# Optimization experiments

Hardware: AMD Instinct MI355X
Metric: run time of the kernel (lower is better)

The kernel has to match this reference:

```python
import jax, jax.numpy as jnp
import numpy as np

HEADS = 8
EPS = 1e-5


def layernorm(x, g, b):
    mu = jnp.mean(x, axis=-1, keepdims=True)
    var = jnp.mean((x - mu) ** 2, axis=-1, keepdims=True)
    return (x - mu) * jax.lax.rsqrt(var + EPS) * g + b


def setup_inputs() -> dict:
    key = jax.random.key(0)
    ks = jax.random.split(key, 5)
    B, C, H, W = 8, 384, 32, 32
    d = C
    s = 0.02
    return {
        "x": jax.random.normal(ks[0], (B, C, H, W), jnp.float32),
        "ln1_g": jnp.ones((d,), jnp.float32),
        "ln1_b": jnp.zeros((d,), jnp.float32),
        "lna_g": jnp.ones((d,), jnp.float32),
        "lna_b": jnp.zeros((d,), jnp.float32),
        "w_qkv": jax.random.normal(ks[1], (d, 3 * d), jnp.float32) * s,
        "w_out": jax.random.normal(ks[2], (d, d), jnp.float32) * s,
        "ln2_g": jnp.ones((d,), jnp.float32),
        "ln2_b": jnp.zeros((d,), jnp.float32),
        "w1": jax.random.normal(ks[3], (d, 4 * d), jnp.float32) * s,
        "b1": jnp.zeros((4 * d,), jnp.float32),
        "w2": jax.random.normal(ks[4], (4 * d, d), jnp.float32) * s,
        "b2": jnp.zeros((d,), jnp.float32),
    }


def reference(x, ln1_g, ln1_b, lna_g, lna_b, w_qkv, w_out, ln2_g, ln2_b, w1, b1, w2, b2):
    B, C, H, W = x.shape
    d = C
    dh = d // HEADS
    scale = dh ** (-0.5)
    # flatten spatial -> tokens: [B, N, C]
    t = x.reshape(B, C, H * W).transpose(0, 2, 1)

    # --- attention branch (note: double pre-norm, as in original) ---
    a = layernorm(t, ln1_g, ln1_b)
    a = layernorm(a, lna_g, lna_b)
    qkv = a @ w_qkv  # [B, N, 3d]
    q, k, v = jnp.split(qkv, 3, axis=-1)
    q = q.reshape(B, -1, HEADS, dh).transpose(0, 2, 1, 3)  # b h n d
    k = k.reshape(B, -1, HEADS, dh).transpose(0, 2, 1, 3)
    v = v.reshape(B, -1, HEADS, dh).transpose(0, 2, 1, 3)
    dots = jnp.einsum("bhnd,bhmd->bhnm", q, k) * scale
    attn = jax.nn.softmax(dots, axis=-1)
    o = jnp.einsum("bhnm,bhmd->bhnd", attn, v)
    o = o.transpose(0, 2, 1, 3).reshape(B, -1, d)
    t = t + o @ w_out

    # --- MLP branch (exact GELU, as torch nn.GELU default) ---
    m = layernorm(t, ln2_g, ln2_b)
    m = jax.nn.gelu(m @ w1 + b1, approximate=False) @ w2 + b2
    t = t + m

    return t.transpose(0, 2, 1).reshape(B, C, H, W)
```

## Files before the change

### kernel.cpp

```cpp
#include <hip/hip_runtime.h>
#include <math.h>

#define NTOK 1024
#define DM   384
#define NHEAD 8
#define DH   48
#define BATCH 8
#define NROWS (BATCH * NTOK)
#define SC2   (0.14433756729740643f * 1.4426950408889634f)

typedef __attribute__((ext_vector_type(8))) _Float16 f16x8;
typedef __attribute__((ext_vector_type(2))) __fp16 fp16x2_raw;
typedef __attribute__((ext_vector_type(4))) float f32x4;

#define ASYNC16(gp, lp) __builtin_amdgcn_global_load_lds( \
    (const __attribute__((address_space(1))) void*)(gp),  \
    (__attribute__((address_space(3))) void*)(lp), 16, 0, 0)

__device__ __forceinline__ unsigned int pkh(float a, float b) {
    union { fp16x2_raw h; unsigned int u; } cv;
    cv.h = __builtin_amdgcn_cvt_pkrtz(a, b);
    return cv.u;
}

__device__ __forceinline__ float gelu_fast(float v) {
    const float u = v * (0.7978845608f + 0.0356774081f * v * v);
    const float e = exp2f(u * 2.885390082f);
    return v * e / (e + 1.0f);
}

__global__ __launch_bounds__(256) void prep_kernel(const float* __restrict__ x,
                                                   const float* __restrict__ ln1_g,
                                                   const float* __restrict__ ln1_b,
                                                   const float* __restrict__ lna_g,
                                                   const float* __restrict__ lna_b,
                                                   float* __restrict__ t,
                                                   _Float16* __restrict__ a_h,
                                                   const float* __restrict__ wqkv,
                                                   const float* __restrict__ wout,
                                                   const float* __restrict__ w1,
                                                   const float* __restrict__ w2,
                                                   _Float16* __restrict__ wqkvT,
                                                   _Float16* __restrict__ woutT,
                                                   _Float16* __restrict__ w1T,
                                                   _Float16* __restrict__ w2T) {
    __shared__ float Ts[32][389];
    const int bid = blockIdx.x;
    const int tid = threadIdx.x;

    if (bid >= 256) {
        float (*tile)[33] = (float(*)[33])&Ts[0][0];
        const int wb = bid - 256;
        const float* W; _Float16* Wt; int K, N, nx, tt;
        if (wb < 432)       { W = wqkv; Wt = wqkvT; K = 384;  N = 1152; nx = 36; tt = wb; }
        else if (wb < 576)  { W = wout; Wt = woutT; K = 384;  N = 384;  nx = 12; tt = wb - 432; }
        else if (wb < 1152) { W = w1;   Wt = w1T;   K = 384;  N = 1536; nx = 48; tt = wb - 576; }
        else                { W = w2;   Wt = w2T;   K = 1536; N = 384;  nx = 12; tt = wb - 1152; }
        const int n0 = (tt % nx) * 32, k0 = (tt / nx) * 32;
        const int tx = tid & 31, ty = tid >> 5;
        #pragma unroll
        for (int i = ty; i < 32; i += 8)
            tile[i][tx] = W[(size_t)(k0 + i) * N + n0 + tx];
        __syncthreads();
        #pragma unroll
        for (int i = ty; i < 32; i += 8)
            Wt[(size_t)(n0 + i) * K + k0 + tx] = (_Float16)tile[tx][i];
        return;
    }

    const int b = bid >> 5, n0 = (bid & 31) * 32;
    const int tx = tid & 31, ty8 = tid >> 5;
    const float* xb = x + (size_t)b * (DM * NTOK);
    #pragma unroll
    for (int c0 = 0; c0 < DM; c0 += 32) {
        #pragma unroll
        for (int i = ty8; i < 32; i += 8)
            Ts[tx][c0 + i] = xb[(size_t)(c0 + i) * NTOK + n0 + tx];
    }
    __syncthreads();

    const int g = tid >> 3, sub = tid & 7;
    const int c0 = sub * 48;
    float xv[48];
    #pragma unroll
    for (int k = 0; k < 12; ++k)
        *(float4*)&xv[k * 4] = *(const float4*)&Ts[g][c0 + k * 4];

    const size_t trow = (size_t)((b << 10) + n0 + g) * DM;
    float s = 0.0f, sq = 0.0f;
    #pragma unroll
    for (int k = 0; k < 12; ++k)
        *(float4*)&t[trow + c0 + k * 4] = *(const float4*)&xv[k * 4];
    #pragma unroll
    for (int j = 0; j < 48; ++j) { s += xv[j]; sq += xv[j] * xv[j]; }
    s += __shfl_xor(s, 1, 64); sq += __shfl_xor(sq, 1, 64);
    s += __shfl_xor(s, 2, 64); sq += __shfl_xor(sq, 2, 64);
    s += __shfl_xor(s, 4, 64); sq += __shfl_xor(sq, 4, 64);
    float mu = s * (1.0f / DM);
    float var = fmaxf(sq * (1.0f / DM) - mu * mu, 0.0f);
    float r1 = rsqrtf(var + 1e-5f);

    float s2 = 0.0f, q2 = 0.0f;
    #pragma unroll
    for (int k = 0; k < 12; ++k) {
        const float4 gk = *(const float4*)&ln1_g[c0 + k * 4];
        const float4 bk = *(const float4*)&ln1_b[c0 + k * 4];
        float y0 = (xv[k*4+0] - mu) * r1 * gk.x + bk.x;
        float y1 = (xv[k*4+1] - mu) * r1 * gk.y + bk.y;
        float y2 = (xv[k*4+2] - mu) * r1 * gk.z + bk.z;
        float y3 = (xv[k*4+3] - mu) * r1 * gk.w + bk.w;
        xv[k*4+0] = y0; xv[k*4+1] = y1; xv[k*4+2] = y2; xv[k*4+3] = y3;
        s2 += (y0 + y1) + (y2 + y3);
        q2 += (y0*y0 + y1*y1) + (y2*y2 + y3*y3);
    }
    s2 += __shfl_xor(s2, 1, 64); q2 += __shfl_xor(q2, 1, 64);
    s2 += __shfl_xor(s2, 2, 64); q2 += __shfl_xor(q2, 2, 64);
    s2 += __shfl_xor(s2, 4, 64); q2 += __shfl_xor(q2, 4, 64);
    mu = s2 * (1.0f / DM);
    var = fmaxf(q2 * (1.0f / DM) - mu * mu, 0.0f);
    const float r2 = rsqrtf(var + 1e-5f);

    unsigned int d[12];
    #pragma unroll
    for (int k = 0; k < 12; ++k) {
        const float4 gk = *(const float4*)&lna_g[c0 + k * 4];
        const float4 bk = *(const float4*)&lna_b[c0 + k * 4];
        const float y0 = (xv[k*4+0] - mu) * r2 * gk.x + bk.x;
        const float y1 = (xv[k*4+1] - mu) * r2 * gk.y + bk.y;
        const float y2 = (xv[k*4+2] - mu) * r2 * gk.z + bk.z;
        const float y3 = (xv[k*4+3] - mu) * r2 * gk.w + bk.w;
        d[k*2+0] = pkh(y0, y1); d[k*2+1] = pkh(y2, y3);
    }
    unsigned int* op = (unsigned int*)(a_h + trow + c0);
    #pragma unroll
    for (int k = 0; k < 3; ++k)
        *(uint4*)(op + k * 4) = *(const uint4*)&d[k * 4];
}

__global__ __launch_bounds__(256) void ln2_kernel(const float* __restrict__ in,
                                                  const float* __restrict__ gg,
                                                  const float* __restrict__ bb,
                                                  _Float16* __restrict__ outp) {
    const int row = blockIdx.x * 4 + (threadIdx.x >> 6);
    const int lane = threadIdx.x & 63;
    const float* ip = in + (size_t)row * DM + lane * 6;
    float v[6];
    *(float2*)&v[0] = *(const float2*)(ip);
    *(float2*)&v[2] = *(const float2*)(ip + 2);
    *(float2*)&v[4] = *(const float2*)(ip + 4);
    float s = 0.0f, sq = 0.0f;
    #pragma unroll
    for (int j = 0; j < 6; ++j) { s += v[j]; sq += v[j] * v[j]; }
    #pragma unroll
    for (int off = 1; off < 64; off <<= 1) {
        s += __shfl_xor(s, off, 64);
        sq += __shfl_xor(sq, off, 64);
    }
    const float mu = s * (1.0f / DM);
    const float var = fmaxf(sq * (1.0f / DM) - mu * mu, 0.0f);
    const float rs = rsqrtf(var + 1e-5f);
    const float* gp = gg + lane * 6;
    const float* bp = bb + lane * 6;
    float y[6];
    #pragma unroll
    for (int j = 0; j < 6; ++j) y[j] = (v[j] - mu) * rs * gp[j] + bp[j];
    unsigned int* op = (unsigned int*)(outp + (size_t)row * DM + lane * 6);
    op[0] = pkh(y[0], y[1]); op[1] = pkh(y[2], y[3]); op[2] = pkh(y[4], y[5]);
}

template <int EPI, int BN>
__global__ __launch_bounds__(256) void gemm_f16(const _Float16* __restrict__ A,
                                                const _Float16* __restrict__ Bt,
                                                const float* __restrict__ bias,
                                                const float* __restrict__ R,
                                                _Float16* __restrict__ Ch,
                                                float* __restrict__ Cf,
                                                int M, int N, int K) {
    constexpr int NFRAG = BN / 32;
    constexpr int BSTG = BN / 32;
    __shared__ _Float16 As[2][128][64];
    __shared__ _Float16 Bs[2][BN][64];
    const int tid = threadIdx.x;
    const int w = tid >> 6, lane = tid & 63;
    const int l15 = lane & 15, lq = lane >> 4;
    const int bm = blockIdx.y * 128, bn = blockIdx.x * BN;
    const int moff = (w & 1) * 64, noff = (w >> 1) * (BN / 2);

    const int srw = lane >> 3, pp = lane & 7;
    const int c = pp ^ srw;
    const _Float16* Ag[4];
    const _Float16* Bg[BSTG];
    #pragma unroll
    for (int j = 0; j < 4; ++j)
        Ag[j] = A + (size_t)(bm + w * 32 + j * 8 + srw) * K + c * 8;
    #pragma unroll
    for (int j = 0; j < BSTG; ++j)
        Bg[j] = Bt + (size_t)(bn + w * (BN / 4) + j * 8 + srw) * K + c * 8;

    const int octA = ((lq ^ (l15 & 7)) << 4);

    f32x4 acc[4][NFRAG];
    #pragma unroll
    for (int mi = 0; mi < 4; ++mi)
        #pragma unroll
        for (int ni = 0; ni < NFRAG; ++ni) acc[mi][ni] = (f32x4){0.f, 0.f, 0.f, 0.f};

    #pragma unroll
    for (int j = 0; j < 4; ++j) { ASYNC16(Ag[j], &As[0][w * 32 + j * 8][0]); Ag[j] += 64; }
    #pragma unroll
    for (int j = 0; j < BSTG; ++j) { ASYNC16(Bg[j], &Bs[0][w * (BN / 4) + j * 8][0]); Bg[j] += 64; }

    int cur = 0;
    for (int k0 = 64; k0 <= K; k0 += 64) {
        __syncthreads();
        if (k0 < K) {
            #pragma unroll
            for (int j = 0; j < 4; ++j) { ASYNC16(Ag[j], &As[cur ^ 1][w * 32 + j * 8][0]); Ag[j] += 64; }
            #pragma unroll
            for (int j = 0; j < BSTG; ++j) { ASYNC16(Bg[j], &Bs[cur ^ 1][w * (BN / 4) + j * 8][0]); Bg[j] += 64; }
        }
        const char* Ab = (const char*)&As[cur][0][0];
        const char* Bb = (const char*)&Bs[cur][0][0];
        #pragma unroll
        for (int ks = 0; ks < 2; ++ks) {
            const int ox = octA ^ (ks << 6);
            f16x8 af[4], bfr[NFRAG];
            #pragma unroll
            for (int mi = 0; mi < 4; ++mi)
                af[mi] = *(const f16x8*)(Ab + ((moff + mi * 16 + l15) << 7) + ox);
            #pragma unroll
            for (int ni = 0; ni < NFRAG; ++ni)
                bfr[ni] = *(const f16x8*)(Bb + ((noff + ni * 16 + l15) << 7) + ox);
            #pragma unroll
            for (int mi = 0; mi < 4; ++mi)
                #pragma unroll
                for (int ni = 0; ni < NFRAG; ++ni)
                    acc[mi][ni] = __builtin_amdgcn_mfma_f32_16x16x32_f16(af[mi], bfr[ni], acc[mi][ni], 0, 0, 0);
        }
        cur ^= 1;
    }

    #pragma unroll
    for (int mi = 0; mi < 4; ++mi) {
        #pragma unroll
        for (int ni = 0; ni < NFRAG; ++ni) {
            const int col = bn + noff + ni * 16 + l15;
            float bv = 0.0f;
            if (EPI >= 2) bv = bias[col];
            if (EPI == 4) {
                const int row0 = bm + moff + mi * 16 + lq * 4;
                const int b = row0 >> 10, nn = row0 & 1023;
                float4 vv;
                vv.x = acc[mi][ni][0] + bv + R[(size_t)(row0 + 0) * N + col];
                vv.y = acc[mi][ni][1] + bv + R[(size_t)(row0 + 1) * N + col];
                vv.z = acc[mi][ni][2] + bv + R[(size_t)(row0 + 2) * N + col];
                vv.w = acc[mi][ni][3] + bv + R[(size_t)(row0 + 3) * N + col];
                *(float4*)(Cf + (size_t)b * (DM * NTOK) + (size_t)col * NTOK + nn) = vv;
            } else {
                #pragma unroll
                for (int r = 0; r < 4; ++r) {
                    const int row = bm + moff + mi * 16 + lq * 4 + r;
                    const size_t idx = (size_t)row * N + col;
                    float v = acc[mi][ni][r];
                    if (EPI == 2) v = gelu_fast(v + bv);
                    if (EPI == 0 || EPI == 2) Ch[idx] = (_Float16)v;
                    else                      Cf[idx] = v + R[idx];
                }
            }
        }
    }
}

__global__ __launch_bounds__(256) void attn_kernel(const _Float16* __restrict__ qkv,
                                                   _Float16* __restrict__ o) {
    __shared__ _Float16 Ks[2][64][64];
    __shared__ _Float16 Vt[2][48][72];
    __shared__ _Float16 Ps[4][32][72];

    const int tid = threadIdx.x;
    const int w = tid >> 6, lane = tid & 63;
    const int l15 = lane & 15, lq = lane >> 4;
    const int bid = blockIdx.x;
    const int bh = ((bid >> 3) & 7) * 8 + (bid & 7);
    const int qt0 = (bid >> 6) * 128;
    const int h = bh & 7, b = bh >> 3;

    const _Float16* qbase = qkv + (size_t)b * NTOK * 1152 + h * 48;
    const _Float16* kbase = qbase + 384;
    const _Float16* vbase = qbase + 768;

    f16x8 qf[2][2];
    #pragma unroll
    for (int qi = 0; qi < 2; ++qi) {
        const size_t qrow = (size_t)(qt0 + w * 32 + qi * 16 + l15) * 1152;
        #pragma unroll
        for (int ks = 0; ks < 2; ++ks) {
            if (ks == 0 || lq < 2)
                qf[qi][ks] = *(const f16x8*)(qbase + qrow + ks * 32 + lq * 8);
            else
                qf[qi][ks] = (f16x8){(_Float16)0, (_Float16)0, (_Float16)0, (_Float16)0,
                                     (_Float16)0, (_Float16)0, (_Float16)0, (_Float16)0};
        }
    }

    const int srw = lane >> 3, pp = lane & 7;
    const int ck = pp ^ srw;
    const int ckoff = (ck < 6) ? ck * 8 : (ck - 6) * 8;
    const _Float16* Kg = kbase + (size_t)(w * 16 + srw) * 1152 + ckoff;
    const int vtp = tid & 31, vfo = tid >> 5;
    const _Float16* Vg = vbase + (size_t)(vtp * 2) * 1152 + vfo * 8;

    const int octK = ((lq ^ (l15 & 7)) << 4);

    ASYNC16(Kg, &Ks[0][w * 16][0]);
    ASYNC16(Kg + 8 * 1152, &Ks[0][w * 16 + 8][0]);
    Kg += 64 * 1152;
    uint4 va, vb;
    if (vfo < 6) { va = *(const uint4*)Vg; vb = *(const uint4*)(Vg + 1152); }
    Vg += 64 * 1152;

    f32x4 oacc[2][3];
    float lpart[2] = {0.0f, 0.0f};
    #pragma unroll
    for (int qi = 0; qi < 2; ++qi)
        #pragma unroll
        for (int vf = 0; vf < 3; ++vf) oacc[qi][vf] = (f32x4){0.f, 0.f, 0.f, 0.f};

    int cur = 0;
    for (int kt = 0; kt < 16; ++kt) {
        if (vfo < 6) {
            const unsigned short* as = (const unsigned short*)&va;
            const unsigned short* bs = (const unsigned short*)&vb;
            #pragma unroll
            for (int j = 0; j < 8; ++j) {
                const unsigned int dw = (unsigned int)as[j] | ((unsigned int)bs[j] << 16);
                *(unsigned int*)((char*)&Vt[cur][0][0] + (vfo * 8 + j) * 144 + vtp * 4) = dw;
            }
        }
        __syncthreads();
        if (kt < 15) {
            ASYNC16(Kg, &Ks[cur ^ 1][w * 16][0]);
            ASYNC16(Kg + 8 * 1152, &Ks[cur ^ 1][w * 16 + 8][0]);
            Kg += 64 * 1152;
            if (vfo < 6) { va = *(const uint4*)Vg; vb = *(const uint4*)(Vg + 1152); }
            Vg += 64 * 1152;
        }

        f32x4 sacc[2][4];
        #pragma unroll
        for (int qi = 0; qi < 2; ++qi)
            #pragma unroll
            for (int mi = 0; mi < 4; ++mi) sacc[qi][mi] = (f32x4){0.f, 0.f, 0.f, 0.f};
        #pragma unroll
        for (int ks = 0; ks < 2; ++ks) {
            const int ox = octK ^ (ks << 6);
            #pragma unroll
            for (int mi = 0; mi < 4; ++mi) {
                const f16x8 kf = *(const f16x8*)((const char*)&Ks[cur][0][0] + ((mi * 16 + l15) << 7) + ox);
                sacc[0][mi] = __builtin_amdgcn_mfma_f32_16x16x32_f16(kf, qf[0][ks], sacc[0][mi], 0, 0, 0);
                sacc[1][mi] = __builtin_amdgcn_mfma_f32_16x16x32_f16(kf, qf[1][ks], sacc[1][mi], 0, 0, 0);
            }
        }

        #pragma unroll
        for (int qi = 0; qi < 2; ++qi) {
            #pragma unroll
            for (int mi = 0; mi < 4; ++mi) {
                const float p0 = exp2f(sacc[qi][mi][0] * SC2);
                const float p1 = exp2f(sacc[qi][mi][1] * SC2);
                const float p2 = exp2f(sacc[qi][mi][2] * SC2);
                const float p3 = exp2f(sacc[qi][mi][3] * SC2);
                lpart[qi] += (p0 + p1) + (p2 + p3);
                uint2 d;
                d.x = pkh(p0, p1); d.y = pkh(p2, p3);
                *(uint2*)((char*)&Ps[w][0][0] + (qi * 16 + l15) * 144 + (mi * 16 + lq * 4) * 2) = d;
            }
        }
        asm volatile("s_waitcnt lgkmcnt(0)" ::: "memory");

        #pragma unroll
        for (int ks = 0; ks < 2; ++ks) {
            const int kk2 = ks * 64 + lq * 16;
            const f16x8 pf0 = *(const f16x8*)((const char*)&Ps[w][0][0] + l15 * 144 + kk2);
            const f16x8 pf1 = *(const f16x8*)((const char*)&Ps[w][0][0] + (16 + l15) * 144 + kk2);
            #pragma unroll
            for (int vf = 0; vf < 3; ++vf) {
                const f16x8 vv = *(const f16x8*)((const char*)&Vt[cur][0][0] + (vf * 16 + l15) * 144 + kk2);
                oacc[0][vf] = __builtin_amdgcn_mfma_f32_16x16x32_f16(vv, pf0, oacc[0][vf], 0, 0, 0);
                oacc[1][vf] = __builtin_amdgcn_mfma_f32_16x16x32_f16(vv, pf1, oacc[1][vf], 0, 0, 0);
            }
        }
        cur ^= 1;
    }

    #pragma unroll
    for (int qi = 0; qi < 2; ++qi) {
        float ls = lpart[qi];
        ls += __shfl_xor(ls, 16, 64);
        ls += __shfl_xor(ls, 32, 64);
        const float linv = 1.0f / ls;
        _Float16* ob = o + (size_t)(b * NTOK + qt0 + w * 32 + qi * 16 + l15) * DM + h * DH;
        #pragma unroll
        for (int vf = 0; vf < 3; ++vf) {
            uint2 d;
            d.x = pkh(oacc[qi][vf][0] * linv, oacc[qi][vf][1] * linv);
            d.y = pkh(oacc[qi][vf][2] * linv, oacc[qi][vf][3] * linv);
            *(uint2*)(ob + vf * 16 + lq * 4) = d;
        }
    }
}

extern "C" void kernel_launch(void* const* d_in, const int* in_sizes, int n_in,
                              void* d_out, int out_size, void* d_ws, size_t ws_size,
                              hipStream_t stream) {
    const float* x     = (const float*)d_in[0];
    const float* ln1_g = (const float*)d_in[1];
    const float* ln1_b = (const float*)d_in[2];
    const float* lna_g = (const float*)d_in[3];
    const float* lna_b = (const float*)d_in[4];
    const float* w_qkv = (const float*)d_in[5];
    const float* w_out = (const float*)d_in[6];
    const float* ln2_g = (const float*)d_in[7];
    const float* ln2_b = (const float*)d_in[8];
    const float* w1    = (const float*)d_in[9];
    const float* b1    = (const float*)d_in[10];
    const float* w2    = (const float*)d_in[11];
    const float* b2    = (const float*)d_in[12];
    float* out = (float*)d_out;

    char* wsb = (char*)d_ws;
    float* t          = (float*)(wsb);
    _Float16* a_h     = (_Float16*)(wsb + 12582912);
    _Float16* qkv_h   = (_Float16*)(wsb + 18874368);
    _Float16* o_h     = (_Float16*)(wsb + 37748736);
    _Float16* h1_h    = (_Float16*)(wsb + 44040192);
    _Float16* wqkvT   = (_Float16*)(wsb + 69206016);
    _Float16* woutT   = (_Float16*)(wsb + 70090752);
    _Float16* w1T     = (_Float16*)(wsb + 70385664);
    _Float16* w2T     = (_Float16*)(wsb + 71565312);

    prep_kernel<<<256 + 1728, 256, 0, stream>>>(x, ln1_g, ln1_b, lna_g, lna_b, t, a_h,
                                                w_qkv, w_out, w1, w2, wqkvT, woutT, w1T, w2T);
    gemm_f16<0, 128><<<dim3(9, 64), 256, 0, stream>>>(a_h, wqkvT, nullptr, nullptr, qkv_h, nullptr, NROWS, 3 * DM, DM);
    attn_kernel<<<512, 256, 0, stream>>>(qkv_h, o_h);
    gemm_f16<1, 64><<<dim3(6, 64), 256, 0, stream>>>(o_h, woutT, nullptr, t, nullptr, t, NROWS, DM, DM);
    ln2_kernel<<<2048, 256, 0, stream>>>(t, ln2_g, ln2_b, a_h);
    gemm_f16<2, 128><<<dim3(12, 64), 256, 0, stream>>>(a_h, w1T, b1, nullptr, h1_h, nullptr, NROWS, 4 * DM, DM);
    gemm_f16<4, 64><<<dim3(6, 64), 256, 0, stream>>>(h1_h, w2T, b2, t, nullptr, out, NROWS, DM, 4 * DM);
}
```

Measured before the change: 234.6 us.

## Split-K the final MLP GEMM with merge kernel and halve attention query tile

```diff
diff --git a/kernel.cpp b/kernel.cpp
--- a/kernel.cpp
+++ b/kernel.cpp
@@ -186,16 +186,19 @@
     const int bm = blockIdx.y * 128, bn = blockIdx.x * BN;
     const int moff = (w & 1) * 64, noff = (w >> 1) * (BN / 2);
 
+    const int kspan = (EPI == 5) ? (K >> 1) : K;
+    const int zoff = (EPI == 5) ? blockIdx.z * kspan : 0;
+
     const int srw = lane >> 3, pp = lane & 7;
     const int c = pp ^ srw;
     const _Float16* Ag[4];
     const _Float16* Bg[BSTG];
     #pragma unroll
     for (int j = 0; j < 4; ++j)
-        Ag[j] = A + (size_t)(bm + w * 32 + j * 8 + srw) * K + c * 8;
+        Ag[j] = A + (size_t)(bm + w * 32 + j * 8 + srw) * K + zoff + c * 8;
     #pragma unroll
     for (int j = 0; j < BSTG; ++j)
-        Bg[j] = Bt + (size_t)(bn + w * (BN / 4) + j * 8 + srw) * K + c * 8;
+        Bg[j] = Bt + (size_t)(bn + w * (BN / 4) + j * 8 + srw) * K + zoff + c * 8;
 
     const int octA = ((lq ^ (l15 & 7)) << 4);
 
@@ -211,9 +214,9 @@
     for (int j = 0; j < BSTG; ++j) { ASYNC16(Bg[j], &Bs[0][w * (BN / 4) + j * 8][0]); Bg[j] += 64; }
 
     int cur = 0;
-    for (int k0 = 64; k0 <= K; k0 += 64) {
+    for (int k0 = 64; k0 <= kspan; k0 += 64) {
         __syncthreads();
-        if (k0 < K) {
+        if (k0 < kspan) {
             #pragma unroll
             for (int j = 0; j < 4; ++j) { ASYNC16(Ag[j], &As[cur ^ 1][w * 32 + j * 8][0]); Ag[j] += 64; }
             #pragma unroll
@@ -240,67 +243,72 @@
         cur ^= 1;
     }
 
+    float* Cfz = (EPI == 5) ? (Cf + (size_t)blockIdx.z * NROWS * 384) : Cf;
     #pragma unroll
     for (int mi = 0; mi < 4; ++mi) {
         #pragma unroll
         for (int ni = 0; ni < NFRAG; ++ni) {
             const int col = bn + noff + ni * 16 + l15;
             float bv = 0.0f;
-            if (EPI >= 2) bv = bias[col];
-            if (EPI == 4) {
-                const int row0 = bm + moff + mi * 16 + lq * 4;
-                const int b = row0 >> 10, nn = row0 & 1023;
-                float4 vv;
-                vv.x = acc[mi][ni][0] + bv + R[(size_t)(row0 + 0) * N + col];
-                vv.y = acc[mi][ni][1] + bv + R[(size_t)(row0 + 1) * N + col];
-                vv.z = acc[mi][ni][2] + bv + R[(size_t)(row0 + 2) * N + col];
-                vv.w = acc[mi][ni][3] + bv + R[(size_t)(row0 + 3) * N + col];
-                *(float4*)(Cf + (size_t)b * (DM * NTOK) + (size_t)col * NTOK + nn) = vv;
-            } else {
-                #pragma unroll
-                for (int r = 0; r < 4; ++r) {
-                    const int row = bm + moff + mi * 16 + lq * 4 + r;
-                    const size_t idx = (size_t)row * N + col;
-                    float v = acc[mi][ni][r];
-                    if (EPI == 2) v = gelu_fast(v + bv);
-                    if (EPI == 0 || EPI == 2) Ch[idx] = (_Float16)v;
-                    else                      Cf[idx] = v + R[idx];
-                }
+            if (EPI == 2) bv = bias[col];
+            #pragma unroll
+            for (int r = 0; r < 4; ++r) {
+                const int row = bm + moff + mi * 16 + lq * 4 + r;
+                const size_t idx = (size_t)row * N + col;
+                float v = acc[mi][ni][r];
+                if (EPI == 2) v = gelu_fast(v + bv);
+                if (EPI == 0 || EPI == 2) Ch[idx] = (_Float16)v;
+                else if (EPI == 1)        Cf[idx] = v + R[idx];
+                else                      Cfz[idx] = v;
             }
         }
     }
+}
+
+__global__ __launch_bounds__(256) void merge_kernel(const float* __restrict__ p0,
+                                                    const float* __restrict__ p1,
+                                                    const float* __restrict__ t,
+                                                    const float* __restrict__ b2,
+                                                    float* __restrict__ out) {
+    __shared__ float tile[32][33];
+    const int b = blockIdx.z, n0 = blockIdx.y * 32, c0 = blockIdx.x * 32;
+    const int tx = threadIdx.x & 31, ty = threadIdx.x >> 5;
+    const float bv = b2[c0 + tx];
+    #pragma unroll
+    for (int i = ty; i < 32; i += 8) {
+        const size_t idx = (size_t)((b << 10) + n0 + i) * DM + c0 + tx;
+        tile[i][tx] = p0[idx] + p1[idx] + t[idx] + bv;
+    }
+    __syncthreads();
+    #pragma unroll
+    for (int i = ty; i < 32; i += 8)
+        out[(size_t)b * (DM * NTOK) + (size_t)(c0 + i) * NTOK + n0 + tx] = tile[tx][i];
 }
 
 __global__ __launch_bounds__(256) void attn_kernel(const _Float16* __restrict__ qkv,
                                                    _Float16* __restrict__ o) {
     __shared__ _Float16 Ks[2][64][64];
     __shared__ _Float16 Vt[2][48][72];
-    __shared__ _Float16 Ps[4][32][72];
-
+    __shared__ _Float16 Ps[4][16][72];
     const int tid = threadIdx.x;
     const int w = tid >> 6, lane = tid & 63;
     const int l15 = lane & 15, lq = lane >> 4;
     const int bid = blockIdx.x;
     const int bh = ((bid >> 3) & 7) * 8 + (bid & 7);
-    const int qt0 = (bid >> 6) * 128;
+    const int qt0 = (bid >> 6) * 64;
     const int h = bh & 7, b = bh >> 3;
 
     const _Float16* qbase = qkv + (size_t)b * NTOK * 1152 + h * 48;
     const _Float16* kbase = qbase + 384;
     const _Float16* vbase = qbase + 768;
 
-    f16x8 qf[2][2];
-    #pragma unroll
-    for (int qi = 0; qi < 2; ++qi) {
-        const size_t qrow = (size_t)(qt0 + w * 32 + qi * 16 + l15) * 1152;
-        #pragma unroll
-        for (int ks = 0; ks < 2; ++ks) {
-            if (ks == 0 || lq < 2)
-                qf[qi][ks] = *(const f16x8*)(qbase + qrow + ks * 32 + lq * 8);
-            else
-                qf[qi][ks] = (f16x8){(_Float16)0, (_Float16)0, (_Float16)0, (_Float16)0,
-                                     (_Float16)0, (_Float16)0, (_Float16)0, (_Float16)0};
-        }
+    f16x8 qf[2];
+    {
+        const size_t qrow = (size_t)(qt0 + w * 16 + l15) * 1152;
+        qf[0] = *(const f16x8*)(qbase + qrow + lq * 8);
+        if (lq < 2) qf[1] = *(const f16x8*)(qbase + qrow + 32 + lq * 8);
+        else        qf[1] = (f16x8){(_Float16)0, (_Float16)0, (_Float16)0, (_Float16)0,
+                                    (_Float16)0, (_Float16)0, (_Float16)0, (_Float16)0};
     }
 
     const int srw = lane >> 3, pp = lane & 7;
@@ -319,12 +327,10 @@
     if (vfo < 6) { va = *(const uint4*)Vg; vb = *(const uint4*)(Vg + 1152); }
     Vg += 64 * 1152;
 
-    f32x4 oacc[2][3];
-    float lpart[2] = {0.0f, 0.0f};
-    #pragma unroll
-    for (int qi = 0; qi < 2; ++qi)
-        #pragma unroll
-        for (int vf = 0; vf < 3; ++vf) oacc[qi][vf] = (f32x4){0.f, 0.f, 0.f, 0.f};
+    f32x4 oacc[3];
+    float lpart = 0.0f;
+    #pragma unroll
+    for (int vf = 0; vf < 3; ++vf) oacc[vf] = (f32x4){0.f, 0.f, 0.f, 0.f};
 
     int cur = 0;
     for (int kt = 0; kt < 16; ++kt) {
@@ -346,67 +352,55 @@
             Vg += 64 * 1152;
         }
 
-        f32x4 sacc[2][4];
-        #pragma unroll
-        for (int qi = 0; qi < 2; ++qi)
-            #pragma unroll
-            for (int mi = 0; mi < 4; ++mi) sacc[qi][mi] = (f32x4){0.f, 0.f, 0.f, 0.f};
+        f32x4 sacc[4];
+        #pragma unroll
+        for (int mi = 0; mi < 4; ++mi) sacc[mi] = (f32x4){0.f, 0.f, 0.f, 0.f};
         #pragma unroll
         for (int ks = 0; ks < 2; ++ks) {
             const int ox = octK ^ (ks << 6);
             #pragma unroll
             for (int mi = 0; mi < 4; ++mi) {
                 const f16x8 kf = *(const f16x8*)((const char*)&Ks[cur][0][0] + ((mi * 16 + l15) << 7) + ox);
-                sacc[0][mi] = __builtin_amdgcn_mfma_f32_16x16x32_f16(kf, qf[0][ks], sacc[0][mi], 0, 0, 0);
-                sacc[1][mi] = __builtin_amdgcn_mfma_f32_16x16x32_f16(kf, qf[1][ks], sacc[1][mi], 0, 0, 0);
+                sacc[mi] = __builtin_amdgcn_mfma_f32_16x16x32_f16(kf, qf[ks], sacc[mi], 0, 0, 0);
             }
         }
 
         #pragma unroll
-        for (int qi = 0; qi < 2; ++qi) {
-            #pragma unroll
-            for (int mi = 0; mi < 4; ++mi) {
-                const float p0 = exp2f(sacc[qi][mi][0] * SC2);
-                const float p1 = exp2f(sacc[qi][mi][1] * SC2);
-                const float p2 = exp2f(sacc[qi][mi][2] * SC2);
-                const float p3 = exp2f(sacc[qi][mi][3] * SC2);
-                lpart[qi] += (p0 + p1) + (p2 + p3);
-                uint2 d;
-                d.x = pkh(p0, p1); d.y = pkh(p2, p3);
-                *(uint2*)((char*)&Ps[w][0][0] + (qi * 16 + l15) * 144 + (mi * 16 + lq * 4) * 2) = d;
-            }
+        for (int mi = 0; mi < 4; ++mi) {
+            const float p0 = exp2f(sacc[mi][0] * SC2);
+            const float p1 = exp2f(sacc[mi][1] * SC2);
+            const float p2 = exp2f(sacc[mi][2] * SC2);
+            const float p3 = exp2f(sacc[mi][3] * SC2);
+            lpart += (p0 + p1) + (p2 + p3);
+            uint2 d;
+            d.x = pkh(p0, p1); d.y = pkh(p2, p3);
+            *(uint2*)((char*)&Ps[w][0][0] + l15 * 144 + (mi * 16 + lq * 4) * 2) = d;
         }
         asm volatile("s_waitcnt lgkmcnt(0)" ::: "memory");
 
         #pragma unroll
         for (int ks = 0; ks < 2; ++ks) {
             const int kk2 = ks * 64 + lq * 16;
-            const f16x8 pf0 = *(const f16x8*)((const char*)&Ps[w][0][0] + l15 * 144 + kk2);
-            const f16x8 pf1 = *(const f16x8*)((const char*)&Ps[w][0][0] + (16 + l15) * 144 + kk2);
+            const f16x8 pf = *(const f16x8*)((const char*)&Ps[w][0][0] + l15 * 144 + kk2);
             #pragma unroll
             for (int vf = 0; vf < 3; ++vf) {
                 const f16x8 vv = *(const f16x8*)((const char*)&Vt[cur][0][0] + (vf * 16 + l15) * 144 + kk2);
-                oacc[0][vf] = __builtin_amdgcn_mfma_f32_16x16x32_f16(vv, pf0, oacc[0][vf], 0, 0, 0);
-                oacc[1][vf] = __builtin_amdgcn_mfma_f32_16x16x32_f16(vv, pf1, oacc[1][vf], 0, 0, 0);
+                oacc[vf] = __builtin_amdgcn_mfma_f32_16x16x32_f16(vv, pf, oacc[vf], 0, 0, 0);
             }
         }
         cur ^= 1;
     }
 
-    #pragma unroll
-    for (int qi = 0; qi < 2; ++qi) {
-        float ls = lpart[qi];
-        ls += __shfl_xor(ls, 16, 64);
-        ls += __shfl_xor(ls, 32, 64);
-        const float linv = 1.0f / ls;
-        _Float16* ob = o + (size_t)(b * NTOK + qt0 + w * 32 + qi * 16 + l15) * DM + h * DH;
-        #pragma unroll
-        for (int vf = 0; vf < 3; ++vf) {
-            uint2 d;
-            d.x = pkh(oacc[qi][vf][0] * linv, oacc[qi][vf][1] * linv);
-            d.y = pkh(oacc[qi][vf][2] * linv, oacc[qi][vf][3] * linv);
-            *(uint2*)(ob + vf * 16 + lq * 4) = d;
-        }
+    lpart += __shfl_xor(lpart, 16, 64);
+    lpart += __shfl_xor(lpart, 32, 64);
+    const float linv = 1.0f / lpart;
+    _Float16* ob = o + (size_t)(b * NTOK + qt0 + w * 16 + l15) * DM + h * DH;
+    #pragma unroll
+    for (int vf = 0; vf < 3; ++vf) {
+        uint2 d;
+        d.x = pkh(oacc[vf][0] * linv, oacc[vf][1] * linv);
+        d.y = pkh(oacc[vf][2] * linv, oacc[vf][3] * linv);
+        *(uint2*)(ob + vf * 16 + lq * 4) = d;
     }
 }
 
@@ -438,13 +432,15 @@
     _Float16* woutT   = (_Float16*)(wsb + 70090752);
     _Float16* w1T     = (_Float16*)(wsb + 70385664);
     _Float16* w2T     = (_Float16*)(wsb + 71565312);
+    float* p01        = (float*)(wsb + 72744960);
 
     prep_kernel<<<256 + 1728, 256, 0, stream>>>(x, ln1_g, ln1_b, lna_g, lna_b, t, a_h,
                                                 w_qkv, w_out, w1, w2, wqkvT, woutT, w1T, w2T);
     gemm_f16<0, 128><<<dim3(9, 64), 256, 0, stream>>>(a_h, wqkvT, nullptr, nullptr, qkv_h, nullptr, NROWS, 3 * DM, DM);
-    attn_kernel<<<512, 256, 0, stream>>>(qkv_h, o_h);
+    attn_kernel<<<1024, 256, 0, stream>>>(qkv_h, o_h);
     gemm_f16<1, 64><<<dim3(6, 64), 256, 0, stream>>>(o_h, woutT, nullptr, t, nullptr, t, NROWS, DM, DM);
     ln2_kernel<<<2048, 256, 0, stream>>>(t, ln2_g, ln2_b, a_h);
     gemm_f16<2, 128><<<dim3(12, 64), 256, 0, stream>>>(a_h, w1T, b1, nullptr, h1_h, nullptr, NROWS, 4 * DM, DM);
-    gemm_f16<4, 64><<<dim3(6, 64), 256, 0, stream>>>(h1_h, w2T, b2, t, nullptr, out, NROWS, DM, 4 * DM);
-}
+    gemm_f16<5, 64><<<dim3(6, 64, 2), 256, 0, stream>>>(h1_h, w2T, nullptr, nullptr, nullptr, p01, NROWS, DM, 4 * DM);
+    merge_kernel<<<dim3(12, 32, 8), 256, 0, stream>>>(p01, p01 + (size_t)NROWS * DM, t, b2, out);
+}
```

Measured after the change: 246.4 us. +5.1%, slower.
